# Kernel tuning notes

Hardware: AMD Instinct MI355X
Metric: run time of the kernel (lower is better)

## Reference

```python
import jax, jax.numpy as jnp
import numpy as np

N = 50000
E = 400000
IN_DIM = 256
HEADS = 4
C = 64          # out_channels per head
HC = HEADS * C  # 256
OUT_DIM = 32
NEG_SLOPE = 0.2


def setup_inputs() -> dict:
    key = jax.random.key(0)
    ks = jax.random.split(key, 16)
    s = lambda fan_in: 1.0 / np.sqrt(fan_in)
    return {
        "x": jax.random.normal(ks[0], (N, IN_DIM), jnp.float32),
        "edge_index": jax.random.randint(ks[1], (2, E), 0, N, jnp.int64),
        # conv1 (lin_l == lin_r, shared)
        "W1": jax.random.normal(ks[2], (IN_DIM, HC), jnp.float32) * s(IN_DIM),
        "b1": jnp.zeros((HC,), jnp.float32),
        "att1": jax.random.normal(ks[3], (HEADS, C), jnp.float32) * s(C),
        # conv2
        "W2": jax.random.normal(ks[4], (HC, HC), jnp.float32) * s(HC),
        "b2": jnp.zeros((HC,), jnp.float32),
        "att2": jax.random.normal(ks[5], (HEADS, C), jnp.float32) * s(C),
        # post_mp: Linear(HC, C_hidden=64) -> Linear(64, OUT_DIM)
        "Wp1": jax.random.normal(ks[6], (HC, C), jnp.float32) * s(HC),
        "bp1": jnp.zeros((C,), jnp.float32),
        "Wp2": jax.random.normal(ks[7], (C, OUT_DIM), jnp.float32) * s(C),
        "bp2": jnp.zeros((OUT_DIM,), jnp.float32),
    }


def _gatv2_layer(x, src, dst, W, b, att):
    # shared lin_l == lin_r, so x_source == x_target projection
    h = (x @ W + b).reshape(-1, HEADS, C)          # [N, H, C]
    x_j = h[src]                                    # source features per edge [E, H, C]
    x_i = h[dst]                                    # target features per edge [E, H, C]
    e = jax.nn.leaky_relu(x_i + x_j, NEG_SLOPE)     # [E, H, C]
    alpha = jnp.einsum('ehc,hc->eh', e, att)        # [E, H]
    # segment softmax grouped by target node (dst)
    amax = jax.ops.segment_max(alpha, dst, num_segments=N)   # [N, H]
    ex = jnp.exp(alpha - amax[dst])
    denom = jax.ops.segment_sum(ex, dst, num_segments=N)     # [N, H]
    alpha = ex / (denom[dst] + 1e-16)
    out = jax.ops.segment_sum(x_j * alpha[:, :, None], dst, num_segments=N)  # [N, H, C]
    return out.reshape(-1, HC)


def reference(x, edge_index, W1, b1, att1, W2, b2, att2, Wp1, bp1, Wp2, bp2):
    src, dst = edge_index[0], edge_index[1]
    h = jax.nn.relu(_gatv2_layer(x, src, dst, W1, b1, att1))
    h = jax.nn.relu(_gatv2_layer(h, src, dst, W2, b2, att2))
    out = (h @ Wp1 + bp1) @ Wp2 + bp2
    return jax.nn.sigmoid(out)
```

## Files before the change

kernel.cpp:

```cpp
#include <hip/hip_runtime.h>
#include <math.h>

#define HC 256
#define NEG_SLOPE 0.2f
#define CAP 64

typedef __attribute__((ext_vector_type(2))) _Float16 h16x2;
typedef __attribute__((ext_vector_type(4))) _Float16 h16x4;
typedef __attribute__((ext_vector_type(8))) _Float16 f16x8;
typedef __attribute__((ext_vector_type(4))) float f32x4;

__device__ __forceinline__ unsigned short f2h16(float f) {
  _Float16 x = (_Float16)f;
  return __builtin_bit_cast(unsigned short, x);
}
__device__ __forceinline__ float h2f(unsigned short u) {
  _Float16 x = __builtin_bit_cast(_Float16, u);
  return (float)x;
}

__device__ __forceinline__ int detect64(const int* e) {
  int v = e[2 * (threadIdx.x & 63) + 1];
  return (__ballot(v != 0) == 0ULL) ? 1 : 0;
}

__device__ __forceinline__ int edge_val(const void* p, int is64, long long idx) {
  return is64 ? (int)((const long long*)p)[idx] : ((const int*)p)[idx];
}

__global__ __launch_bounds__(256) void prep_fill_kernel(
    const float* __restrict__ W1, const float* __restrict__ W2,
    const float* __restrict__ Wp1, const float* __restrict__ bp1,
    const float* __restrict__ Wp2, const float* __restrict__ bp2,
    unsigned short* __restrict__ W1t, unsigned short* __restrict__ W2t,
    unsigned short* __restrict__ Wft16, float* __restrict__ bf,
    const void* __restrict__ edges, int* __restrict__ cursor,
    int* __restrict__ csr_src, int E) {
  const int b = blockIdx.x, t = threadIdx.x;
  if (b < 512) {
    int n = b & 255;
    const float* W = (b >> 8) ? W2 : W1;
    unsigned short* Wt = (b >> 8) ? W2t : W1t;
    Wt[(size_t)n * 256 + t] = f2h16(W[(size_t)t * 256 + n]);
    return;
  }
  if (b == 512) {
    float acc[32];
#pragma unroll
    for (int o = 0; o < 32; ++o) acc[o] = 0.f;
    for (int ll = 0; ll < 64; ++ll) {
      float w1 = Wp1[t * 64 + ll];
#pragma unroll
      for (int o = 0; o < 32; ++o) acc[o] += w1 * Wp2[ll * 32 + o];
    }
#pragma unroll
    for (int o = 0; o < 32; ++o) Wft16[o * 256 + t] = f2h16(acc[o]);
    if (t < 32) {
      float s = bp2[t];
      for (int ll = 0; ll < 64; ++ll) s += bp1[ll] * Wp2[ll * 32 + t];
      bf[t] = s;
    }
    return;
  }
  int is64 = detect64((const int*)edges);
  int base = (b - 513) * 1024;
#pragma unroll
  for (int k = 0; k < 4; ++k) {
    int e = base + k * 256 + t;
    if (e < E) {
      int src = edge_val(edges, is64, e);
      int dst = edge_val(edges, is64, (long long)E + e);
      int p = atomicAdd(&cursor[dst], 1);
      if (p < CAP) csr_src[dst * CAP + p] = src;
    }
  }
}

template <bool AF32>
__device__ __forceinline__ void gemm_body(
    const void* __restrict__ Araw, const unsigned short* __restrict__ Bt,
    const float* __restrict__ bias, unsigned short* __restrict__ C, int M,
    int orig, int nwg) {
  __shared__ __align__(16) short As[2][128 * 64];
  __shared__ __align__(16) short Bs[2][128 * 64];
  const int q = nwg >> 3, r = nwg & 7;
  const int xcd = orig & 7, pos = orig >> 3;
  const int logical = (xcd < r ? xcd * (q + 1) : r * (q + 1) + (xcd - r) * q) + pos;
  const int m0 = (logical >> 1) * 128, n0 = (logical & 1) * 128;

  const int t = threadIdx.x;
  const int l = t & 63, w = t >> 6;
  const int wr = w >> 1, wc = w & 1;
  const int l15 = l & 15, lg = l >> 4;

  const int ccs = ((t & 7) ^ ((t >> 3) & 7)) * 8;
  int rowL[4], ldsI[4];
#pragma unroll
  for (int i = 0; i < 4; ++i) {
    rowL[i] = i * 32 + (t >> 3);
    ldsI[i] = (i * 256 + t) * 8;
  }

  f32x4 acc[4][4];
#pragma unroll
  for (int m = 0; m < 4; ++m)
#pragma unroll
    for (int n = 0; n < 4; ++n) acc[m][n] = (f32x4){0.f, 0.f, 0.f, 0.f};

  uint4 ra[4], rb[4];
  auto LOAD = [&](int ks) {
    int k0 = ks * 64;
#pragma unroll
    for (int i = 0; i < 4; ++i) {
      int ar = m0 + rowL[i];
      ar = (ar < M) ? ar : (M - 1);
      if (AF32) {
        const float* A = (const float*)Araw;
        float4 fa = *(const float4*)(A + (size_t)ar * 256 + k0 + ccs);
        float4 fb = *(const float4*)(A + (size_t)ar * 256 + k0 + ccs + 4);
        ra[i].x = f2h16(fa.x) | ((unsigned)f2h16(fa.y) << 16);
        ra[i].y = f2h16(fa.z) | ((unsigned)f2h16(fa.w) << 16);
        ra[i].z = f2h16(fb.x) | ((unsigned)f2h16(fb.y) << 16);
        ra[i].w = f2h16(fb.z) | ((unsigned)f2h16(fb.w) << 16);
      } else {
        const unsigned short* A = (const unsigned short*)Araw;
        ra[i] = *(const uint4*)(A + (size_t)ar * 256 + k0 + ccs);
      }
      rb[i] = *(const uint4*)(Bt + (size_t)(n0 + rowL[i]) * 256 + k0 + ccs);
    }
  };
  auto WRITE = [&](int buf) {
#pragma unroll
    for (int i = 0; i < 4; ++i) {
      *(uint4*)&As[buf][ldsI[i]] = ra[i];
      *(uint4*)&Bs[buf][ldsI[i]] = rb[i];
    }
  };

  int rA[4], rB[4];
#pragma unroll
  for (int m = 0; m < 4; ++m) rA[m] = (wr * 64 + m * 16 + l15) * 64;
#pragma unroll
  for (int n = 0; n < 4; ++n) rB[n] = (wc * 64 + n * 16 + l15) * 64;
  const int swz0 = ((0 * 4 + lg) ^ (l & 7)) * 8;
  const int swz1 = ((1 * 4 + lg) ^ (l & 7)) * 8;

  LOAD(0);
  WRITE(0);
  __syncthreads();
  for (int ks = 0; ks < 4; ++ks) {
    if (ks < 3) LOAD(ks + 1);
    const int buf = ks & 1;
#pragma unroll
    for (int kk = 0; kk < 2; ++kk) {
      const int swz = kk ? swz1 : swz0;
      f16x8 a[4], b[4];
#pragma unroll
      for (int m = 0; m < 4; ++m) a[m] = *(const f16x8*)&As[buf][rA[m] + swz];
#pragma unroll
      for (int n = 0; n < 4; ++n) b[n] = *(const f16x8*)&Bs[buf][rB[n] + swz];
#pragma unroll
      for (int m = 0; m < 4; ++m)
#pragma unroll
        for (int n = 0; n < 4; ++n)
          acc[m][n] = __builtin_amdgcn_mfma_f32_16x16x32_f16(a[m], b[n], acc[m][n], 0, 0, 0);
    }
    if (ks < 3) WRITE((ks + 1) & 1);
    __syncthreads();
  }

  float bcol[4];
#pragma unroll
  for (int n = 0; n < 4; ++n) bcol[n] = bias[n0 + wc * 64 + n * 16 + l15];
#pragma unroll
  for (int m = 0; m < 4; ++m) {
    int baseRow = m0 + wr * 64 + m * 16 + lg * 4;
#pragma unroll
    for (int rr = 0; rr < 4; ++rr) {
      int row = baseRow + rr;
      if (row < M) {
#pragma unroll
        for (int n = 0; n < 4; ++n)
          C[(size_t)row * 256 + n0 + wc * 64 + n * 16 + l15] = f2h16(acc[m][n][rr] + bcol[n]);
      }
    }
  }
}

__global__ __launch_bounds__(256) void gemm1_kernel(
    const float* __restrict__ x, const unsigned short* __restrict__ W1t,
    const float* __restrict__ b1, unsigned short* __restrict__ h, int M) {
  gemm_body<true>((const void*)x, W1t, b1, h, M, blockIdx.x, gridDim.x);
}

__global__ __launch_bounds__(256) void gemm2_kernel(
    const unsigned short* __restrict__ A, const unsigned short* __restrict__ W2t,
    const float* __restrict__ b2, unsigned short* __restrict__ h, int M) {
  gemm_body<false>((const void*)A, W2t, b2, h, M, blockIdx.x, gridDim.x);
}

__global__ __launch_bounds__(256) void gat_fused_kernel(
    const unsigned short* __restrict__ h, const float* __restrict__ att,
    const int* __restrict__ deg, const int* __restrict__ csr_src,
    unsigned short* __restrict__ out16, int N) {
  const int wid = threadIdx.x >> 6, ln = threadIdx.x & 63;
  const int node = blockIdx.x * 4 + wid;
  if (node >= N) return;
  const float4 attv = *(const float4*)(att + ln * 4);
  const h16x2 at_lo = {(_Float16)attv.x, (_Float16)attv.y};
  const h16x2 at_hi = {(_Float16)attv.z, (_Float16)attv.w};
  const _Float16 kns = (_Float16)NEG_SLOPE;
  const h16x4 k4 = {kns, kns, kns, kns};
  const h16x4 hi4 = *(const h16x4*)(h + (size_t)node * HC + ln * 4);
  const int beg = node * CAP;
  const int cnt = min(__builtin_amdgcn_readfirstlane(deg[node]), CAP);
  const int end = beg + cnt;
  const size_t vo = (size_t)ln * 4;

  float d = 0.f;
  float4 S = make_float4(0.f, 0.f, 0.f, 0.f);

  int e0 = beg;
  for (; e0 + 8 <= end; e0 += 8) {
    h16x4 hj[8];
    float p[8];
#pragma unroll
    for (int c = 0; c < 8; ++c) {
      int j = __builtin_amdgcn_readfirstlane(csr_src[e0 + c]);
      hj[c] = *(const h16x4*)(h + (size_t)j * HC + vo);
    }
#pragma unroll
    for (int c = 0; c < 8; ++c) {
      h16x4 s4 = hi4 + hj[c];
      h16x4 l4 = __builtin_elementwise_max(s4, s4 * k4);
      float pp = __builtin_amdgcn_fdot2(l4.lo, at_lo,
                 __builtin_amdgcn_fdot2(l4.hi, at_hi, 0.f, false), false);
#pragma unroll
      for (int off = 1; off < 16; off <<= 1) pp += __shfl_xor(pp, off, 64);
      p[c] = pp;
    }
#pragma unroll
    for (int c = 0; c < 8; ++c) {
      float wgt = __expf(p[c]);
      d += wgt;
      S.x += wgt * (float)hj[c].x;
      S.y += wgt * (float)hj[c].y;
      S.z += wgt * (float)hj[c].z;
      S.w += wgt * (float)hj[c].w;
    }
  }
  if (e0 < end) {
    const int tcnt = end - e0;
    h16x4 hj[8];
#pragma unroll
    for (int c = 0; c < 8; ++c) {
      int j = __builtin_amdgcn_readfirstlane(csr_src[min(e0 + c, end - 1)]);
      hj[c] = *(const h16x4*)(h + (size_t)j * HC + vo);
    }
#pragma unroll
    for (int c = 0; c < 8; ++c) {
      if (c < tcnt) {
        h16x4 s4 = hi4 + hj[c];
        h16x4 l4 = __builtin_elementwise_max(s4, s4 * k4);
        float pp = __builtin_amdgcn_fdot2(l4.lo, at_lo,
                   __builtin_amdgcn_fdot2(l4.hi, at_hi, 0.f, false), false);
#pragma unroll
        for (int off = 1; off < 16; off <<= 1) pp += __shfl_xor(pp, off, 64);
        float wgt = __expf(pp);
        d += wgt;
        S.x += wgt * (float)hj[c].x;
        S.y += wgt * (float)hj[c].y;
        S.z += wgt * (float)hj[c].z;
        S.w += wgt * (float)hj[c].w;
      }
    }
  }

  float inv = (d > 0.f) ? (1.f / d) : 0.f;
  ushort4 ub;
  ub.x = f2h16(fmaxf(S.x * inv, 0.f));
  ub.y = f2h16(fmaxf(S.y * inv, 0.f));
  ub.z = f2h16(fmaxf(S.z * inv, 0.f));
  ub.w = f2h16(fmaxf(S.w * inv, 0.f));
  *(ushort4*)(out16 + (size_t)node * HC + vo) = ub;
}

__global__ __launch_bounds__(256) void post_kernel(
    const unsigned short* __restrict__ g, const unsigned short* __restrict__ Wft16,
    const float* __restrict__ bf, float* __restrict__ out, int M) {
  const int l = threadIdx.x & 63, w = threadIdx.x >> 6;
  const int r0 = blockIdx.x * 256 + w * 64;
  const int l15 = l & 15, lg = l >> 4;

  f16x8 bfrag[2][8];
#pragma unroll
  for (int n = 0; n < 2; ++n)
#pragma unroll
    for (int ks = 0; ks < 8; ++ks)
      bfrag[n][ks] = *(const f16x8*)(Wft16 + (size_t)(n * 16 + l15) * 256 + ks * 32 + lg * 8);

  float b0 = bf[l15], b1 = bf[16 + l15];

  f32x4 acc[4][2];
#pragma unroll
  for (int m = 0; m < 4; ++m)
#pragma unroll
    for (int n = 0; n < 2; ++n) acc[m][n] = (f32x4){0.f, 0.f, 0.f, 0.f};

#pragma unroll
  for (int m = 0; m < 4; ++m) {
    int row = r0 + m * 16 + l15;
    row = (row < M) ? row : (M - 1);
    const unsigned short* gp = g + (size_t)row * 256 + lg * 8;
#pragma unroll
    for (int ks = 0; ks < 8; ++ks) {
      f16x8 a = *(const f16x8*)(gp + ks * 32);
      acc[m][0] = __builtin_amdgcn_mfma_f32_16x16x32_f16(a, bfrag[0][ks], acc[m][0], 0, 0, 0);
      acc[m][1] = __builtin_amdgcn_mfma_f32_16x16x32_f16(a, bfrag[1][ks], acc[m][1], 0, 0, 0);
    }
  }

#pragma unroll
  for (int m = 0; m < 4; ++m) {
    int baseRow = r0 + m * 16 + lg * 4;
#pragma unroll
    for (int rr = 0; rr < 4; ++rr) {
      int row = baseRow + rr;
      if (row < M) {
        float v0 = acc[m][0][rr] + b0;
        float v1 = acc[m][1][rr] + b1;
        out[(size_t)row * 32 + l15]      = 1.f / (1.f + __expf(-v0));
        out[(size_t)row * 32 + 16 + l15] = 1.f / (1.f + __expf(-v1));
      }
    }
  }
}

extern "C" void kernel_launch(void* const* d_in, const int* in_sizes, int n_in,
                              void* d_out, int out_size, void* d_ws, size_t ws_size,
                              hipStream_t stream) {
  const float* x    = (const float*)d_in[0];
  const void*  ei   = d_in[1];
  const float* W1   = (const float*)d_in[2];
  const float* b1   = (const float*)d_in[3];
  const float* att1 = (const float*)d_in[4];
  const float* W2   = (const float*)d_in[5];
  const float* b2   = (const float*)d_in[6];
  const float* att2 = (const float*)d_in[7];
  const float* Wp1  = (const float*)d_in[8];
  const float* bp1  = (const float*)d_in[9];
  const float* Wp2  = (const float*)d_in[10];
  const float* bp2  = (const float*)d_in[11];
  const int N = in_sizes[0] / 256;
  const int E = in_sizes[1] / 2;
  float* outp = (float*)d_out;

  char* ws = (char*)d_ws;
  size_t off = 0;
  auto alloc = [&](size_t bytes) {
    char* p = ws + off;
    off = (off + bytes + 255) & ~(size_t)255;
    return p;
  };
  unsigned short* h16  = (unsigned short*)alloc((size_t)N * 256 * 2);
  unsigned short* a16  = (unsigned short*)alloc((size_t)N * 256 * 2);
  unsigned short* g16  = (unsigned short*)alloc((size_t)N * 256 * 2);
  int*   cursor   = (int*)alloc((size_t)N * 4);
  int*   csr      = (int*)alloc((size_t)N * CAP * 4);
  unsigned short* W1t = (unsigned short*)alloc(256 * 256 * 2);
  unsigned short* W2t = (unsigned short*)alloc(256 * 256 * 2);
  unsigned short* Wft16 = (unsigned short*)alloc(32 * 256 * 2);
  float* bfv      = (float*)alloc(32 * 4);

  const int CBe = (E + 1023) / 1024;
  const int mt  = (N + 127) / 128;
  const int GB  = mt * 2;

  hipMemsetAsync(cursor, 0, (size_t)N * 4, stream);
  hipLaunchKernelGGL(prep_fill_kernel, dim3(513 + CBe), dim3(256), 0, stream,
                     W1, W2, Wp1, bp1, Wp2, bp2, W1t, W2t, Wft16, bfv,
                     ei, cursor, csr, E);
  hipLaunchKernelGGL(gemm1_kernel, dim3(GB), dim3(256), 0, stream, x, W1t, b1, h16, N);
  hipLaunchKernelGGL(gat_fused_kernel, dim3((N + 3) / 4), dim3(256), 0, stream,
                     h16, att1, cursor, csr, a16, N);
  hipLaunchKernelGGL(gemm2_kernel, dim3(GB), dim3(256), 0, stream, a16, W2t, b2, h16, N);
  hipLaunchKernelGGL(gat_fused_kernel, dim3((N + 3) / 4), dim3(256), 0, stream,
                     h16, att2, cursor, csr, g16, N);
  hipLaunchKernelGGL(post_kernel, dim3((N + 255) / 256), dim3(256), 0, stream,
                     g16, Wft16, bfv, outp, N);
}
```

Measured before the change: 167.9 us.

## Split each GAT wavefront into two half-waves processing alternate edges with 8-channel loads

The fused GAT aggregation kernel now splits each 64-lane wavefront into two 32-lane halves. Each half handles alternate edges and loads 8 fp16 channels per lane (16-byte loads) instead of 4. This halves the per-head shuffle reduction depth and the number of serial iterations per edge batch. Attention weights are prescaled by log2(e) so the softmax can use exp2 directly. The cost is a cross-half shuffle reduction of 9 values at the end, plus per-lane index loads in place of readfirstlane scalar loads.

Measured after the change: 169.6 us. No clear change (+1.0%).

```diff
diff --git a/kernel.cpp b/kernel.cpp
--- a/kernel.cpp
+++ b/kernel.cpp
@@ -206,83 +206,94 @@
   const int wid = threadIdx.x >> 6, ln = threadIdx.x & 63;
   const int node = blockIdx.x * 4 + wid;
   if (node >= N) return;
-  const float4 attv = *(const float4*)(att + ln * 4);
-  const h16x2 at_lo = {(_Float16)attv.x, (_Float16)attv.y};
-  const h16x2 at_hi = {(_Float16)attv.z, (_Float16)attv.w};
+  const int s = ln >> 5, q = ln & 31;
+  const int ch0 = q * 8;
+  const float LOG2E = 1.4426950408889634f;
+  const float4 a0 = *(const float4*)(att + ch0);
+  const float4 a1 = *(const float4*)(att + ch0 + 4);
+  const h16x2 atA = {(_Float16)(a0.x * LOG2E), (_Float16)(a0.y * LOG2E)};
+  const h16x2 atB = {(_Float16)(a0.z * LOG2E), (_Float16)(a0.w * LOG2E)};
+  const h16x2 atC = {(_Float16)(a1.x * LOG2E), (_Float16)(a1.y * LOG2E)};
+  const h16x2 atD = {(_Float16)(a1.z * LOG2E), (_Float16)(a1.w * LOG2E)};
   const _Float16 kns = (_Float16)NEG_SLOPE;
-  const h16x4 k4 = {kns, kns, kns, kns};
-  const h16x4 hi4 = *(const h16x4*)(h + (size_t)node * HC + ln * 4);
+  const f16x8 k8 = {kns, kns, kns, kns, kns, kns, kns, kns};
+  const f16x8 hi8 = *(const f16x8*)(h + (size_t)node * HC + ch0);
   const int beg = node * CAP;
   const int cnt = min(__builtin_amdgcn_readfirstlane(deg[node]), CAP);
   const int end = beg + cnt;
-  const size_t vo = (size_t)ln * 4;
 
   float d = 0.f;
-  float4 S = make_float4(0.f, 0.f, 0.f, 0.f);
+  float S[8] = {0.f, 0.f, 0.f, 0.f, 0.f, 0.f, 0.f, 0.f};
+
+  auto score = [&](const f16x8& hj) -> float {
+    f16x8 s8 = hi8 + hj;
+    f16x8 l8 = __builtin_elementwise_max(s8, s8 * k8);
+    float pp = __builtin_amdgcn_fdot2(l8.lo.lo, atA,
+               __builtin_amdgcn_fdot2(l8.lo.hi, atB,
+               __builtin_amdgcn_fdot2(l8.hi.lo, atC,
+               __builtin_amdgcn_fdot2(l8.hi.hi, atD, 0.f, false), false), false), false);
+    pp += __shfl_xor(pp, 1, 64);
+    pp += __shfl_xor(pp, 2, 64);
+    pp += __shfl_xor(pp, 4, 64);
+    return pp;
+  };
+  auto accum = [&](const f16x8& hj, float wgt) {
+    d += wgt;
+#pragma unroll
+    for (int k = 0; k < 8; ++k) S[k] += wgt * (float)hj[k];
+  };
 
   int e0 = beg;
   for (; e0 + 8 <= end; e0 += 8) {
-    h16x4 hj[8];
-    float p[8];
-#pragma unroll
-    for (int c = 0; c < 8; ++c) {
-      int j = __builtin_amdgcn_readfirstlane(csr_src[e0 + c]);
-      hj[c] = *(const h16x4*)(h + (size_t)j * HC + vo);
-    }
-#pragma unroll
-    for (int c = 0; c < 8; ++c) {
-      h16x4 s4 = hi4 + hj[c];
-      h16x4 l4 = __builtin_elementwise_max(s4, s4 * k4);
-      float pp = __builtin_amdgcn_fdot2(l4.lo, at_lo,
-                 __builtin_amdgcn_fdot2(l4.hi, at_hi, 0.f, false), false);
-#pragma unroll
-      for (int off = 1; off < 16; off <<= 1) pp += __shfl_xor(pp, off, 64);
-      p[c] = pp;
-    }
-#pragma unroll
-    for (int c = 0; c < 8; ++c) {
-      float wgt = __expf(p[c]);
-      d += wgt;
-      S.x += wgt * (float)hj[c].x;
-      S.y += wgt * (float)hj[c].y;
-      S.z += wgt * (float)hj[c].z;
-      S.w += wgt * (float)hj[c].w;
-    }
+    int jv[4];
+#pragma unroll
+    for (int r2 = 0; r2 < 4; ++r2) jv[r2] = csr_src[e0 + 2 * r2 + s];
+    f16x8 hj[4];
+#pragma unroll
+    for (int r2 = 0; r2 < 4; ++r2)
+      hj[r2] = *(const f16x8*)(h + (size_t)jv[r2] * HC + ch0);
+    float p[4];
+#pragma unroll
+    for (int r2 = 0; r2 < 4; ++r2) p[r2] = score(hj[r2]);
+#pragma unroll
+    for (int r2 = 0; r2 < 4; ++r2) accum(hj[r2], __builtin_amdgcn_exp2f(p[r2]));
   }
   if (e0 < end) {
     const int tcnt = end - e0;
-    h16x4 hj[8];
-#pragma unroll
-    for (int c = 0; c < 8; ++c) {
-      int j = __builtin_amdgcn_readfirstlane(csr_src[min(e0 + c, end - 1)]);
-      hj[c] = *(const h16x4*)(h + (size_t)j * HC + vo);
-    }
-#pragma unroll
-    for (int c = 0; c < 8; ++c) {
-      if (c < tcnt) {
-        h16x4 s4 = hi4 + hj[c];
-        h16x4 l4 = __builtin_elementwise_max(s4, s4 * k4);
-        float pp = __builtin_amdgcn_fdot2(l4.lo, at_lo,
-                   __builtin_amdgcn_fdot2(l4.hi, at_hi, 0.f, false), false);
-#pragma unroll
-        for (int off = 1; off < 16; off <<= 1) pp += __shfl_xor(pp, off, 64);
-        float wgt = __expf(pp);
-        d += wgt;
-        S.x += wgt * (float)hj[c].x;
-        S.y += wgt * (float)hj[c].y;
-        S.z += wgt * (float)hj[c].z;
-        S.w += wgt * (float)hj[c].w;
+    int jv[4];
+    f16x8 hj[4];
+#pragma unroll
+    for (int r2 = 0; r2 < 4; ++r2) {
+      jv[r2] = csr_src[min(e0 + 2 * r2 + s, end - 1)];
+      hj[r2] = *(const f16x8*)(h + (size_t)jv[r2] * HC + ch0);
+    }
+#pragma unroll
+    for (int r2 = 0; r2 < 4; ++r2) {
+      if (2 * r2 < tcnt) {
+        float pp = score(hj[r2]);
+        bool valid = (2 * r2 + s) < tcnt;
+        float wgt = valid ? __builtin_amdgcn_exp2f(pp) : 0.f;
+        accum(hj[r2], wgt);
       }
     }
   }
 
-  float inv = (d > 0.f) ? (1.f / d) : 0.f;
-  ushort4 ub;
-  ub.x = f2h16(fmaxf(S.x * inv, 0.f));
-  ub.y = f2h16(fmaxf(S.y * inv, 0.f));
-  ub.z = f2h16(fmaxf(S.z * inv, 0.f));
-  ub.w = f2h16(fmaxf(S.w * inv, 0.f));
-  *(ushort4*)(out16 + (size_t)node * HC + vo) = ub;
+  d += __shfl_xor(d, 32, 64);
+#pragma unroll
+  for (int k = 0; k < 8; ++k) S[k] += __shfl_xor(S[k], 32, 64);
+
+  if (s == 0) {
+    float inv = (d > 0.f) ? (1.f / d) : 0.f;
+    unsigned r[8];
+#pragma unroll
+    for (int k = 0; k < 8; ++k) r[k] = f2h16(fmaxf(S[k] * inv, 0.f));
+    uint4 u;
+    u.x = r[0] | (r[1] << 16);
+    u.y = r[2] | (r[3] << 16);
+    u.z = r[4] | (r[5] << 16);
+    u.w = r[6] | (r[7] << 16);
+    *(uint4*)(out16 + (size_t)node * HC + ch0) = u;
+  }
 }
 
 __global__ __launch_bounds__(256) void post_kernel(
```
